# Kernel tuning notes

Hardware: AMD Instinct MI355X
Metric: run time of the kernel (lower is better)

The kernel has to match this reference:

```python
import jax, jax.numpy as jnp
import numpy as np

N, C, H, W = 8, 3, 720, 1280


def setup_inputs() -> dict:
    key = jax.random.key(0)
    k1, k2 = jax.random.split(key)
    image = jax.random.normal(k1, (N, C, H, W), dtype=jnp.float32)
    # scale flow so integer truncation gives real displacements (and collisions)
    flow = jax.random.normal(k2, (N, 2, H, W), dtype=jnp.float32) * 20.0
    return {"image": image, "flow": flow}


def _warp_fw(image, flow):
    n, c, h, w = image.shape
    hw = h * w
    # flat source mesh coordinates (same for all batches)
    mx = jnp.broadcast_to(jnp.arange(w, dtype=jnp.int32)[None, :], (h, w)).reshape(-1)
    my = jnp.broadcast_to(jnp.arange(h, dtype=jnp.int32)[:, None], (h, w)).reshape(-1)
    fx = flow[:, 0].reshape(n, hw)
    fy = flow[:, 1].reshape(n, hw)
    # torch .long() truncates toward zero; astype(int32) matches
    wx = jnp.clip(mx[None, :] + fx.astype(jnp.int32), 0, w - 1)
    wy = jnp.clip(my[None, :] + fy.astype(jnp.int32), 0, h - 1)
    tgt = wy * w + wx  # (n, hw) linear target index
    v = fx * fx + fy * fy
    sortidx = jnp.argsort(v, axis=1)  # (n, hw) ascending
    ranks = jnp.arange(hw, dtype=jnp.int32)

    def per_batch(sortidx_i, tgt_i):
        # rank[p] = position of source pixel p in the sorted write order
        rank = jnp.zeros((hw,), jnp.int32).at[sortidx_i].set(ranks)
        # winning (max) rank at each target location; -1 = hole
        best = jnp.full((hw,), -1, jnp.int32).at[tgt_i].max(rank)
        covered = best >= 0
        # winning source pixel index = sortidx[best_rank]
        src = jnp.take(sortidx_i, jnp.clip(best, 0, hw - 1))
        return src, covered

    src, covered = jax.vmap(per_batch)(sortidx, tgt)  # (n, hw) each
    img_flat = image.reshape(n, c, hw)
    gathered = jnp.take_along_axis(
        img_flat, jnp.broadcast_to(src[:, None, :], (n, c, hw)), axis=2
    )
    out = jnp.where(covered[:, None, :], gathered, 0.0)
    return out.reshape(n, c, h, w)


def reference(image, flow):
    return _warp_fw(image, flow)
```

## Files before the change

### kernel.cpp

```cpp
#include <hip/hip_runtime.h>
#include <cstdint>

constexpr int N_ = 8;
constexpr int C_ = 3;
constexpr int H_ = 720;
constexpr int W_ = 1280;
constexpr int HW = H_ * W_;

constexpr int TW = 128;
constexpr int TH = 64;
constexpr int M_ = 96;
constexpr int NTX = W_ / TW;
constexpr int NTY = (H_ + TH - 1) / TH;
constexpr int BLK = 512;
constexpr int OCAP = 4096;

typedef float vf4 __attribute__((ext_vector_type(4)));

struct Outlier { unsigned long long key; int n; int tgt; };

__device__ __forceinline__ unsigned long long make_key(float fx, float fy, int p) {
    float v = __fadd_rn(__fmul_rn(fx, fx), __fmul_rn(fy, fy));
    return ((unsigned long long)__float_as_uint(v) << 32) | (unsigned int)(p + 1);
}

__global__ __launch_bounds__(256) void outlier_kernel(
    const float* __restrict__ flow,
    unsigned long long* __restrict__ ocnt,
    Outlier* __restrict__ olist) {
    int idx = blockIdx.x * 256 + threadIdx.x;
    int n = idx / (HW / 4);
    int p0 = (idx - n * (HW / 4)) * 4;
    const float* f = flow + (size_t)n * 2 * HW;
    vf4 fx4 = *(const vf4*)(f + p0);
    vf4 fy4 = *(const vf4*)(f + HW + p0);
    float fxs[4] = {fx4.x, fx4.y, fx4.z, fx4.w};
    float fys[4] = {fy4.x, fy4.y, fy4.z, fy4.w};
    int y = p0 / W_;
    int x0 = p0 - y * W_;
    #pragma unroll
    for (int i = 0; i < 4; ++i) {
        int dx = (int)fxs[i];
        int dy = (int)fys[i];
        if (dx > M_ || dx < -M_ || dy > M_ || dy < -M_) {
            int wx = min(max(x0 + i + dx, 0), W_ - 1);
            int wy = min(max(y + dy, 0), H_ - 1);
            unsigned long long o = atomicAdd(ocnt, 1ULL);
            if (o < (unsigned long long)OCAP) {
                Outlier e;
                e.key = make_key(fxs[i], fys[i], p0 + i);
                e.n = n;
                e.tgt = wy * W_ + wx;
                olist[o] = e;
            }
        }
    }
}

__global__ __launch_bounds__(BLK, 4) void warp_tile_kernel(
    const float* __restrict__ image,
    const float* __restrict__ flow,
    const unsigned long long* __restrict__ ocnt,
    const Outlier* __restrict__ olist,
    float* __restrict__ out) {
    __shared__ unsigned long long lkey[TH * TW];
    int tx0 = blockIdx.x * TW;
    int ty0 = blockIdx.y * TH;
    int n   = blockIdx.z;
    int th_eff = min(TH, H_ - ty0);
    int tid = threadIdx.x;

    for (int i = tid; i < TH * TW; i += BLK) lkey[i] = 0ULL;
    __syncthreads();

    int wy0 = max(0, ty0 - M_), wy1 = min(H_, ty0 + th_eff + M_);
    int wx0 = max(0, tx0 - M_), wx1 = min(W_, tx0 + TW + M_);
    int gx = (wx1 - wx0) >> 2;
    int total = gx * (wy1 - wy0);
    const float* fx_p = flow + (size_t)n * 2 * HW;
    const float* fy_p = fx_p + HW;

    for (int g = tid; g < total; g += BLK) {
        int gy = g / gx;
        int gxx = g - gy * gx;
        int y = wy0 + gy;
        int x4 = wx0 + 4 * gxx;
        int pbase = y * W_ + x4;
        vf4 fx4 = *(const vf4*)(fx_p + pbase);
        vf4 fy4 = *(const vf4*)(fy_p + pbase);
        float fxs[4] = {fx4.x, fx4.y, fx4.z, fx4.w};
        float fys[4] = {fy4.x, fy4.y, fy4.z, fy4.w};
        #pragma unroll
        for (int i = 0; i < 4; ++i) {
            float fx = fxs[i], fy = fys[i];
            int wx = x4 + i + (int)fx;
            int wy = y + (int)fy;
            wx = min(max(wx, 0), W_ - 1);
            wy = min(max(wy, 0), H_ - 1);
            int lx = wx - tx0, ly = wy - ty0;
            if ((unsigned)lx < (unsigned)TW && (unsigned)ly < (unsigned)th_eff) {
                atomicMax(&lkey[ly * TW + lx], make_key(fx, fy, pbase + i));
            }
        }
    }
    __syncthreads();

    unsigned long long craw = *ocnt;
    int cnt = (int)(craw > (unsigned long long)OCAP ? OCAP : craw);
    for (int o = tid; o < cnt; o += BLK) {
        Outlier e = olist[o];
        if (e.n == n) {
            int ey = e.tgt / W_, ex = e.tgt - (e.tgt / W_) * W_;
            int lx = ex - tx0, ly = ey - ty0;
            if ((unsigned)lx < (unsigned)TW && (unsigned)ly < (unsigned)th_eff)
                atomicMax(&lkey[ly * TW + lx], e.key);
        }
    }
    __syncthreads();

    const float* img_n = image + (size_t)n * C_ * HW;
    float* out_n = out + (size_t)n * C_ * HW;
    int q4 = th_eff * (TW / 4);
    for (int s = tid; s < q4; s += BLK) {
        int r = s >> 5;
        int cg = s & 31;
        int lp = r * TW + cg * 4;
        unsigned long long k0 = lkey[lp],     k1 = lkey[lp + 1];
        unsigned long long k2 = lkey[lp + 2], k3 = lkey[lp + 3];
        int s0 = (int)(unsigned int)(k0 & 0xffffffffULL) - 1;
        int s1 = (int)(unsigned int)(k1 & 0xffffffffULL) - 1;
        int s2 = (int)(unsigned int)(k2 & 0xffffffffULL) - 1;
        int s3 = (int)(unsigned int)(k3 & 0xffffffffULL) - 1;
        int op = (ty0 + r) * W_ + tx0 + cg * 4;
        #pragma unroll
        for (int c = 0; c < C_; ++c) {
            const float* pl = img_n + (size_t)c * HW;
            vf4 o;
            o.x = k0 ? pl[s0] : 0.0f;
            o.y = k1 ? pl[s1] : 0.0f;
            o.z = k2 ? pl[s2] : 0.0f;
            o.w = k3 ? pl[s3] : 0.0f;
            __builtin_nontemporal_store(o, (vf4*)(out_n + (size_t)c * HW + op));
        }
    }
}

extern "C" void kernel_launch(void* const* d_in, const int* in_sizes, int n_in,
                              void* d_out, int out_size, void* d_ws, size_t ws_size,
                              hipStream_t stream) {
    const float* image = (const float*)d_in[0];
    const float* flow  = (const float*)d_in[1];
    float* out = (float*)d_out;

    unsigned long long* ocnt = (unsigned long long*)d_ws;
    Outlier* olist = (Outlier*)((char*)d_ws + 64);

    (void)hipMemsetAsync(ocnt, 0, sizeof(unsigned long long), stream);

    int k0_blocks = (N_ * HW / 4) / 256;
    outlier_kernel<<<k0_blocks, 256, 0, stream>>>(flow, ocnt, olist);

    dim3 grid(NTX, NTY, N_);
    warp_tile_kernel<<<grid, BLK, 0, stream>>>(image, flow, ocnt, olist, out);
}
```

Before: 336.0 us.

## Shrink halo, segment outliers per batch, and restructure tile flow scan

Reduces the halo margin from 96 to 64 so each tile scans a smaller flow window, and pushes more pixels through a per-batch outlier list. The list is now split into 8 segments with their own counters, so tiles read only their batch's entries and skip the batch check. The flow scan is remapped to a fixed 64-column by 8-row thread layout with no per-iteration division. The 3D grid is flattened with the batch index in the low bits. The trade-offs are more outliers to process per tile and a larger outlier buffer. Correctness now depends on each batch's outliers fitting in the 16384-entry segment.

```diff
diff --git a/kernel.cpp b/kernel.cpp
--- a/kernel.cpp
+++ b/kernel.cpp
@@ -9,15 +9,15 @@
 
 constexpr int TW = 128;
 constexpr int TH = 64;
-constexpr int M_ = 96;
+constexpr int M_ = 64;
 constexpr int NTX = W_ / TW;
 constexpr int NTY = (H_ + TH - 1) / TH;
 constexpr int BLK = 512;
-constexpr int OCAP = 4096;
+constexpr int OSEG = 16384;
 
 typedef float vf4 __attribute__((ext_vector_type(4)));
 
-struct Outlier { unsigned long long key; int n; int tgt; };
+struct Outlier { unsigned long long key; int tgt; int pad; };
 
 __device__ __forceinline__ unsigned long long make_key(float fx, float fy, int p) {
     float v = __fadd_rn(__fmul_rn(fx, fx), __fmul_rn(fy, fy));
@@ -45,13 +45,13 @@
         if (dx > M_ || dx < -M_ || dy > M_ || dy < -M_) {
             int wx = min(max(x0 + i + dx, 0), W_ - 1);
             int wy = min(max(y + dy, 0), H_ - 1);
-            unsigned long long o = atomicAdd(ocnt, 1ULL);
-            if (o < (unsigned long long)OCAP) {
+            unsigned long long o = atomicAdd(&ocnt[n], 1ULL);
+            if (o < (unsigned long long)OSEG) {
                 Outlier e;
                 e.key = make_key(fxs[i], fys[i], p0 + i);
-                e.n = n;
                 e.tgt = wy * W_ + wx;
-                olist[o] = e;
+                e.pad = 0;
+                olist[n * OSEG + o] = e;
             }
         }
     }
@@ -64,9 +64,13 @@
     const Outlier* __restrict__ olist,
     float* __restrict__ out) {
     __shared__ unsigned long long lkey[TH * TW];
-    int tx0 = blockIdx.x * TW;
-    int ty0 = blockIdx.y * TH;
-    int n   = blockIdx.z;
+    int bid = blockIdx.x;
+    int n    = bid & 7;
+    int tile = bid >> 3;
+    int tyi = tile / NTX;
+    int txi = tile - tyi * NTX;
+    int tx0 = txi * TW;
+    int ty0 = tyi * TH;
     int th_eff = min(TH, H_ - ty0);
     int tid = threadIdx.x;
 
@@ -75,46 +79,44 @@
 
     int wy0 = max(0, ty0 - M_), wy1 = min(H_, ty0 + th_eff + M_);
     int wx0 = max(0, tx0 - M_), wx1 = min(W_, tx0 + TW + M_);
-    int gx = (wx1 - wx0) >> 2;
-    int total = gx * (wy1 - wy0);
     const float* fx_p = flow + (size_t)n * 2 * HW;
     const float* fy_p = fx_p + HW;
 
-    for (int g = tid; g < total; g += BLK) {
-        int gy = g / gx;
-        int gxx = g - gy * gx;
-        int y = wy0 + gy;
-        int x4 = wx0 + 4 * gxx;
-        int pbase = y * W_ + x4;
-        vf4 fx4 = *(const vf4*)(fx_p + pbase);
-        vf4 fy4 = *(const vf4*)(fy_p + pbase);
-        float fxs[4] = {fx4.x, fx4.y, fx4.z, fx4.w};
-        float fys[4] = {fy4.x, fy4.y, fy4.z, fy4.w};
-        #pragma unroll
-        for (int i = 0; i < 4; ++i) {
-            float fx = fxs[i], fy = fys[i];
-            int wx = x4 + i + (int)fx;
-            int wy = y + (int)fy;
-            wx = min(max(wx, 0), W_ - 1);
-            wy = min(max(wy, 0), H_ - 1);
-            int lx = wx - tx0, ly = wy - ty0;
-            if ((unsigned)lx < (unsigned)TW && (unsigned)ly < (unsigned)th_eff) {
-                atomicMax(&lkey[ly * TW + lx], make_key(fx, fy, pbase + i));
+    int x4   = wx0 + ((tid & 63) << 2);
+    int rowg = tid >> 6;
+    if (x4 < wx1) {
+        #pragma unroll 2
+        for (int y = wy0 + rowg; y < wy1; y += 8) {
+            int pbase = y * W_ + x4;
+            vf4 fx4 = *(const vf4*)(fx_p + pbase);
+            vf4 fy4 = *(const vf4*)(fy_p + pbase);
+            float fxs[4] = {fx4.x, fx4.y, fx4.z, fx4.w};
+            float fys[4] = {fy4.x, fy4.y, fy4.z, fy4.w};
+            #pragma unroll
+            for (int i = 0; i < 4; ++i) {
+                float fx = fxs[i], fy = fys[i];
+                int wx = x4 + i + (int)fx;
+                int wy = y + (int)fy;
+                wx = min(max(wx, 0), W_ - 1);
+                wy = min(max(wy, 0), H_ - 1);
+                int lx = wx - tx0, ly = wy - ty0;
+                if ((unsigned)lx < (unsigned)TW && (unsigned)ly < (unsigned)th_eff) {
+                    atomicMax(&lkey[ly * TW + lx], make_key(fx, fy, pbase + i));
+                }
             }
         }
     }
     __syncthreads();
 
-    unsigned long long craw = *ocnt;
-    int cnt = (int)(craw > (unsigned long long)OCAP ? OCAP : craw);
+    unsigned long long craw = ocnt[n];
+    int cnt = (int)(craw > (unsigned long long)OSEG ? OSEG : craw);
+    const Outlier* seg = olist + n * OSEG;
     for (int o = tid; o < cnt; o += BLK) {
-        Outlier e = olist[o];
-        if (e.n == n) {
-            int ey = e.tgt / W_, ex = e.tgt - (e.tgt / W_) * W_;
-            int lx = ex - tx0, ly = ey - ty0;
-            if ((unsigned)lx < (unsigned)TW && (unsigned)ly < (unsigned)th_eff)
-                atomicMax(&lkey[ly * TW + lx], e.key);
-        }
+        Outlier e = seg[o];
+        int ey = e.tgt / W_, ex = e.tgt - ey * W_;
+        int lx = ex - tx0, ly = ey - ty0;
+        if ((unsigned)lx < (unsigned)TW && (unsigned)ly < (unsigned)th_eff)
+            atomicMax(&lkey[ly * TW + lx], e.key);
     }
     __syncthreads();
 
@@ -155,11 +157,11 @@
     unsigned long long* ocnt = (unsigned long long*)d_ws;
     Outlier* olist = (Outlier*)((char*)d_ws + 64);
 
-    (void)hipMemsetAsync(ocnt, 0, sizeof(unsigned long long), stream);
+    (void)hipMemsetAsync(ocnt, 0, 8 * sizeof(unsigned long long), stream);
 
     int k0_blocks = (N_ * HW / 4) / 256;
     outlier_kernel<<<k0_blocks, 256, 0, stream>>>(flow, ocnt, olist);
 
-    dim3 grid(NTX, NTY, N_);
-    warp_tile_kernel<<<grid, BLK, 0, stream>>>(image, flow, ocnt, olist, out);
+    warp_tile_kernel<<<N_ * NTX * NTY, BLK, 0, stream>>>(
+        image, flow, ocnt, olist, out);
 }
```

Result: slower. 469.1 us (+39.6%).
